# Kernel tuning notes

Measured on AMD Instinct MI355X. Metric: run time of the kernel, lower is better.

Reference implementation:

```python
import jax, jax.numpy as jnp
import numpy as np

# competition weights: first target weighted 0.3, remaining four 0.175 each
W = jnp.asarray([0.3, 0.175, 0.175, 0.175, 0.175], dtype=jnp.float32)


def setup_inputs() -> dict:
    key = jax.random.key(0)
    k1, k2 = jax.random.split(key)
    N = 4194304
    # y_true must have nonzero column means (it is a divisor), so use uniform(0,1)+0.5
    y_true = jax.random.uniform(k1, (N, 5), dtype=jnp.float32) + 0.5
    y_preds = jax.random.uniform(k2, (N, 5), dtype=jnp.float32)
    return {"y_true": y_true, "y_preds": y_preds}


def reference(y_true, y_preds):
    # op = mean_n( |y_true - y_preds| @ (w / mean(y_true, axis=0)) )
    col_mean = jnp.mean(y_true, axis=0)            # [5]
    scaled_w = W / col_mean                        # [5]
    per_row = jnp.abs(y_true - y_preds) @ scaled_w  # [N]
    return jnp.mean(per_row)                       # scalar
```

## Files before the change

### kernel.cpp

```cpp
#include <hip/hip_runtime.h>
#include <math.h>


#define RBLOCKS 2048
#define RTHREADS 256

__global__ __launch_bounds__(RTHREADS) void regress_reduce(
    const float* __restrict__ yt, const float* __restrict__ yp,
    float* __restrict__ partials, long long nrows) {
  float s[5] = {0.f, 0.f, 0.f, 0.f, 0.f};
  float a[5] = {0.f, 0.f, 0.f, 0.f, 0.f};

  const long long tid = (long long)blockIdx.x * blockDim.x + threadIdx.x;
  const long long stride = (long long)gridDim.x * blockDim.x;
  const long long ngroups = nrows >> 2;

#define ACC(c, tv, pv) { s[c] += (tv); a[c] += fabsf((tv) - (pv)); }

  for (long long g = tid; g < ngroups; g += stride) {
    const float4* t4 = (const float4*)(yt + g * 20);
    const float4* p4 = (const float4*)(yp + g * 20);
    float4 t0 = t4[0], t1 = t4[1], t2 = t4[2], t3 = t4[3], t4v = t4[4];
    float4 p0 = p4[0], p1 = p4[1], p2 = p4[2], p3 = p4[3], p4v = p4[4];

    ACC(0, t0.x, p0.x)  ACC(1, t0.y, p0.y)  ACC(2, t0.z, p0.z)  ACC(3, t0.w, p0.w)
    ACC(4, t1.x, p1.x)  ACC(0, t1.y, p1.y)  ACC(1, t1.z, p1.z)  ACC(2, t1.w, p1.w)
    ACC(3, t2.x, p2.x)  ACC(4, t2.y, p2.y)  ACC(0, t2.z, p2.z)  ACC(1, t2.w, p2.w)
    ACC(2, t3.x, p3.x)  ACC(3, t3.y, p3.y)  ACC(4, t3.z, p3.z)  ACC(0, t3.w, p3.w)
    ACC(1, t4v.x, p4v.x) ACC(2, t4v.y, p4v.y) ACC(3, t4v.z, p4v.z) ACC(4, t4v.w, p4v.w)
  }

  const long long rem_start = ngroups << 2;
  const long long rem = nrows - rem_start;
  if (tid < rem) {
    const long long r = rem_start + tid;
#pragma unroll
    for (int c = 0; c < 5; ++c) {
      float tv = yt[r * 5 + c];
      ACC(c, tv, yp[r * 5 + c])
    }
  }
#undef ACC

#pragma unroll
  for (int off = 32; off > 0; off >>= 1) {
#pragma unroll
    for (int c = 0; c < 5; ++c) {
      s[c] += __shfl_down(s[c], off, 64);
      a[c] += __shfl_down(a[c], off, 64);
    }
  }

  __shared__ float lds[RTHREADS / 64][10];
  const int lane = threadIdx.x & 63;
  const int wave = threadIdx.x >> 6;
  if (lane == 0) {
#pragma unroll
    for (int c = 0; c < 5; ++c) { lds[wave][c] = s[c]; lds[wave][5 + c] = a[c]; }
  }
  __syncthreads();
  if (threadIdx.x == 0) {
#pragma unroll
    for (int v = 0; v < 10; ++v) {
      float sum = 0.f;
#pragma unroll
      for (int w = 0; w < RTHREADS / 64; ++w) sum += lds[w][v];
      partials[(long long)blockIdx.x * 10 + v] = sum;
    }
  }
}

__global__ __launch_bounds__(256) void regress_finalize(
    const float* __restrict__ partials, int nblocks, float* __restrict__ out) {
  float acc[10] = {0.f, 0.f, 0.f, 0.f, 0.f, 0.f, 0.f, 0.f, 0.f, 0.f};
  for (int b = threadIdx.x; b < nblocks; b += 256) {
#pragma unroll
    for (int v = 0; v < 10; ++v) acc[v] += partials[b * 10 + v];
  }
#pragma unroll
  for (int off = 32; off > 0; off >>= 1) {
#pragma unroll
    for (int v = 0; v < 10; ++v) acc[v] += __shfl_down(acc[v], off, 64);
  }
  __shared__ float lds[4][10];
  const int lane = threadIdx.x & 63;
  const int wave = threadIdx.x >> 6;
  if (lane == 0) {
#pragma unroll
    for (int v = 0; v < 10; ++v) lds[wave][v] = acc[v];
  }
  __syncthreads();
  if (threadIdx.x == 0) {
    const float W[5] = {0.3f, 0.175f, 0.175f, 0.175f, 0.175f};
    float r = 0.f;
#pragma unroll
    for (int c = 0; c < 5; ++c) {
      float sc = lds[0][c] + lds[1][c] + lds[2][c] + lds[3][c];
      float ac = lds[0][5 + c] + lds[1][5 + c] + lds[2][5 + c] + lds[3][5 + c];
      r += W[c] * ac / sc;
    }
    *out = r;
  }
}

extern "C" void kernel_launch(void* const* d_in, const int* in_sizes, int n_in,
                              void* d_out, int out_size, void* d_ws, size_t ws_size,
                              hipStream_t stream) {
  const float* yt = (const float*)d_in[0];
  const float* yp = (const float*)d_in[1];
  const long long nrows = (long long)in_sizes[0] / 5;
  float* partials = (float*)d_ws;

  regress_reduce<<<RBLOCKS, RTHREADS, 0, stream>>>(yt, yp, partials, nrows);
  regress_finalize<<<1, 256, 0, stream>>>(partials, RBLOCKS, (float*)d_out);
}
```

Before: 187.7 us.

## Add fully coalesced size-specialized float4 reduction path with modular column remapping

Adds a fast kernel used when the element count exactly matches grid*block*10*4. In it, each thread issues ten independent float4 loads at grid-stride offsets, so each wave reads contiguous memory instead of every thread reading 80 contiguous bytes on its own. Because the column of each element now depends on the thread and the load index, per-thread accumulators are rotated by tid%5 before a shared-memory tree reduction. The warp-shuffle block reduction is replaced by an LDS tree with many barriers, and the fast path only applies to one exact input size, with a generic row-strided fallback for all other sizes.

```diff
diff --git a/kernel.cpp b/kernel.cpp
--- a/kernel.cpp
+++ b/kernel.cpp
@@ -2,72 +2,83 @@
 #include <math.h>
 
 
-#define RBLOCKS 2048
-#define RTHREADS 256
+#define GRID 2048
+#define BLOCK 256
+#define TTHREADS (GRID * BLOCK)
+#define KLOADS 10
 
-__global__ __launch_bounds__(RTHREADS) void regress_reduce(
+__global__ __launch_bounds__(BLOCK) void regress_reduce_fast(
+    const float4* __restrict__ yt4, const float4* __restrict__ yp4,
+    float* __restrict__ partials) {
+  const int tid = blockIdx.x * BLOCK + threadIdx.x;
+
+  float s[5] = {0.f, 0.f, 0.f, 0.f, 0.f};
+  float a[5] = {0.f, 0.f, 0.f, 0.f, 0.f};
+
+#pragma unroll
+  for (int k = 0; k < KLOADS; ++k) {
+    const float4 tv = yt4[tid + k * TTHREADS];
+    const float4 pv = yp4[tid + k * TTHREADS];
+    const int m0 = (2 * k + 0) % 5;
+    const int m1 = (2 * k + 1) % 5;
+    const int m2 = (2 * k + 2) % 5;
+    const int m3 = (2 * k + 3) % 5;
+    s[m0] += tv.x; a[m0] += fabsf(tv.x - pv.x);
+    s[m1] += tv.y; a[m1] += fabsf(tv.y - pv.y);
+    s[m2] += tv.z; a[m2] += fabsf(tv.z - pv.z);
+    s[m3] += tv.w; a[m3] += fabsf(tv.w - pv.w);
+  }
+
+  __shared__ float red[BLOCK][11];
+  const int t = threadIdx.x;
+  const int rr = tid % 5;
+#pragma unroll
+  for (int m = 0; m < 5; ++m) {
+    int g = m - rr; if (g < 0) g += 5;
+    red[t][g] = s[m];
+    red[t][5 + g] = a[m];
+  }
+  __syncthreads();
+#pragma unroll
+  for (int off = BLOCK / 2; off > 0; off >>= 1) {
+    if (t < off) {
+#pragma unroll
+      for (int v = 0; v < 10; ++v) red[t][v] += red[t + off][v];
+    }
+    __syncthreads();
+  }
+  if (t < 10) partials[blockIdx.x * 10 + t] = red[0][t];
+}
+
+__global__ __launch_bounds__(BLOCK) void regress_reduce_generic(
     const float* __restrict__ yt, const float* __restrict__ yp,
     float* __restrict__ partials, long long nrows) {
   float s[5] = {0.f, 0.f, 0.f, 0.f, 0.f};
   float a[5] = {0.f, 0.f, 0.f, 0.f, 0.f};
-
   const long long tid = (long long)blockIdx.x * blockDim.x + threadIdx.x;
   const long long stride = (long long)gridDim.x * blockDim.x;
-  const long long ngroups = nrows >> 2;
-
-#define ACC(c, tv, pv) { s[c] += (tv); a[c] += fabsf((tv) - (pv)); }
-
-  for (long long g = tid; g < ngroups; g += stride) {
-    const float4* t4 = (const float4*)(yt + g * 20);
-    const float4* p4 = (const float4*)(yp + g * 20);
-    float4 t0 = t4[0], t1 = t4[1], t2 = t4[2], t3 = t4[3], t4v = t4[4];
-    float4 p0 = p4[0], p1 = p4[1], p2 = p4[2], p3 = p4[3], p4v = p4[4];
-
-    ACC(0, t0.x, p0.x)  ACC(1, t0.y, p0.y)  ACC(2, t0.z, p0.z)  ACC(3, t0.w, p0.w)
-    ACC(4, t1.x, p1.x)  ACC(0, t1.y, p1.y)  ACC(1, t1.z, p1.z)  ACC(2, t1.w, p1.w)
-    ACC(3, t2.x, p2.x)  ACC(4, t2.y, p2.y)  ACC(0, t2.z, p2.z)  ACC(1, t2.w, p2.w)
-    ACC(2, t3.x, p3.x)  ACC(3, t3.y, p3.y)  ACC(4, t3.z, p3.z)  ACC(0, t3.w, p3.w)
-    ACC(1, t4v.x, p4v.x) ACC(2, t4v.y, p4v.y) ACC(3, t4v.z, p4v.z) ACC(4, t4v.w, p4v.w)
-  }
-
-  const long long rem_start = ngroups << 2;
-  const long long rem = nrows - rem_start;
-  if (tid < rem) {
-    const long long r = rem_start + tid;
+  for (long long r = tid; r < nrows; r += stride) {
 #pragma unroll
     for (int c = 0; c < 5; ++c) {
       float tv = yt[r * 5 + c];
-      ACC(c, tv, yp[r * 5 + c])
+      s[c] += tv;
+      a[c] += fabsf(tv - yp[r * 5 + c]);
     }
   }
-#undef ACC
-
+  __shared__ float red[BLOCK][11];
+  const int t = threadIdx.x;
 #pragma unroll
-  for (int off = 32; off > 0; off >>= 1) {
+  for (int c = 0; c < 5; ++c) { red[t][c] = s[c]; red[t][5 + c] = a[c]; }
+  __syncthreads();
 #pragma unroll
-    for (int c = 0; c < 5; ++c) {
-      s[c] += __shfl_down(s[c], off, 64);
-      a[c] += __shfl_down(a[c], off, 64);
+  for (int off = BLOCK / 2; off > 0; off >>= 1) {
+    if (t < off) {
+#pragma unroll
+      for (int v = 0; v < 10; ++v) red[t][v] += red[t + off][v];
     }
+    __syncthreads();
   }
-
-  __shared__ float lds[RTHREADS / 64][10];
-  const int lane = threadIdx.x & 63;
-  const int wave = threadIdx.x >> 6;
-  if (lane == 0) {
-#pragma unroll
-    for (int c = 0; c < 5; ++c) { lds[wave][c] = s[c]; lds[wave][5 + c] = a[c]; }
-  }
-  __syncthreads();
-  if (threadIdx.x == 0) {
-#pragma unroll
-    for (int v = 0; v < 10; ++v) {
-      float sum = 0.f;
-#pragma unroll
-      for (int w = 0; w < RTHREADS / 64; ++w) sum += lds[w][v];
-      partials[(long long)blockIdx.x * 10 + v] = sum;
-    }
-  }
+  if (t < 10) partials[blockIdx.x * 10 + t] = red[0][t];
 }
 
 __global__ __launch_bounds__(256) void regress_finalize(
@@ -108,9 +119,15 @@
                               hipStream_t stream) {
   const float* yt = (const float*)d_in[0];
   const float* yp = (const float*)d_in[1];
-  const long long nrows = (long long)in_sizes[0] / 5;
+  const long long nelem = (long long)in_sizes[0];
+  const long long nrows = nelem / 5;
   float* partials = (float*)d_ws;
 
-  regress_reduce<<<RBLOCKS, RTHREADS, 0, stream>>>(yt, yp, partials, nrows);
-  regress_finalize<<<1, 256, 0, stream>>>(partials, RBLOCKS, (float*)d_out);
+  if (nelem == (long long)TTHREADS * KLOADS * 4) {
+    regress_reduce_fast<<<GRID, BLOCK, 0, stream>>>(
+        (const float4*)yt, (const float4*)yp, partials);
+  } else {
+    regress_reduce_generic<<<GRID, BLOCK, 0, stream>>>(yt, yp, partials, nrows);
+  }
+  regress_finalize<<<1, 256, 0, stream>>>(partials, GRID, (float*)d_out);
 }
```

Measured after the change: 187.1 us. Within noise of the previous version (-0.3%).
